# Kernel optimization log

Hardware: AMD Instinct MI355X
Metric: run time of the kernel (lower is better)

Reference implementation:

```python
import jax, jax.numpy as jnp
import numpy as np

N, E, F_IN, HID, H, NCLS, L = 100000, 1600000, 128, 128, 4, 40, 2
C = HID // H  # per-head channels = 32
LN_EPS = 1e-5
SOFTMAX_EPS = 1e-16  # PyG softmax denominator epsilon


def setup_inputs() -> dict:
    key = jax.random.key(0)
    ks = jax.random.split(key, 8)
    s = 1.0 / np.sqrt(F_IN).astype(np.float32)
    return {
        "x": jax.random.normal(ks[0], (N, F_IN), jnp.float32),
        "edge_index": jax.random.randint(ks[1], (2, E), 0, N, jnp.int32),
        "Wq": jax.random.normal(ks[2], (L, F_IN, HID), jnp.float32) * s,
        "bq": jnp.zeros((L, HID), jnp.float32),
        "Wk": jax.random.normal(ks[3], (L, F_IN, HID), jnp.float32) * s,
        "bk": jnp.zeros((L, HID), jnp.float32),
        "Wv": jax.random.normal(ks[4], (L, F_IN, HID), jnp.float32) * s,
        "bv": jnp.zeros((L, HID), jnp.float32),
        "Ws": jax.random.normal(ks[5], (L, F_IN, HID), jnp.float32) * s,
        "bs": jnp.zeros((L, HID), jnp.float32),
        "gamma": jnp.ones((L, HID), jnp.float32),
        "beta": jnp.zeros((L, HID), jnp.float32),
        "Wout": jax.random.normal(ks[6], (HID, NCLS), jnp.float32) * (1.0 / np.sqrt(HID).astype(np.float32)),
        "bout": jnp.zeros((NCLS,), jnp.float32),
    }


def _transformer_conv(x, src, dst, Wq, bq, Wk, bk, Wv, bv, Ws, bs):
    # PyG TransformerConv, concat=False, root_weight=True, beta=False
    n = x.shape[0]
    q = (x @ Wq + bq).reshape(n, H, C)
    k = (x @ Wk + bk).reshape(n, H, C)
    v = (x @ Wv + bv).reshape(n, H, C)
    # per-edge attention logits: [E, H]
    alpha = jnp.einsum('ehc,ehc->eh', q[dst], k[src]) / np.sqrt(C).astype(np.float32)
    # segment softmax over incoming edges of each destination node
    amax = jax.ops.segment_max(alpha, dst, num_segments=n)        # [N, H]
    ex = jnp.exp(alpha - amax[dst])                               # [E, H]
    denom = jax.ops.segment_sum(ex, dst, num_segments=n)         # [N, H]
    w = ex / (denom[dst] + SOFTMAX_EPS)                           # [E, H]
    msg = v[src] * w[:, :, None]                                  # [E, H, C]
    out = jax.ops.segment_sum(msg, dst, num_segments=n)          # [N, H, C]
    out = out.mean(axis=1)                                        # concat=False -> head average, [N, C*?]. Here C*H==HID only via mean over H of C dims -> [N, C]
    # NOTE: concat=False averages heads -> [N, C]; skip proj maps in->C? In PyG, out_channels=hidden here,
    # so lin_* are Linear(in, heads*hidden)... but TransformerConv(in, hidden) means out_channels=hidden/?
    return out


def _conv(x, src, dst, Wq, bq, Wk, bk, Wv, bv, Ws, bs):
    # Faithful version with out_channels = HID per head? No: TransformerConv(in, hidden, heads, concat=False)
    # in PyG uses out_channels=hidden and lin_* : in -> heads*out_channels. To keep HID total width we model
    # per-head dim C = HID // H (standard multi-head factorization with same total width HID).
    n = x.shape[0]
    q = (x @ Wq + bq).reshape(n, H, C)
    k = (x @ Wk + bk).reshape(n, H, C)
    v = (x @ Wv + bv).reshape(n, H, C)
    alpha = jnp.einsum('ehc,ehc->eh', q[dst], k[src]) / np.sqrt(C).astype(np.float32)
    amax = jax.ops.segment_max(alpha, dst, num_segments=n)
    ex = jnp.exp(alpha - amax[dst])
    denom = jax.ops.segment_sum(ex, dst, num_segments=n)
    w = ex / (denom[dst] + SOFTMAX_EPS)
    msg = (v[src] * w[:, :, None]).reshape(-1, H * C)             # [E, HID]
    agg = jax.ops.segment_sum(msg, dst, num_segments=n)          # [N, HID]
    # concat=False -> mean over heads, then broadcast back is not what PyG does; PyG yields [N, out_channels].
    out = agg.reshape(n, H, C).mean(axis=1)                       # [N, C]
    out = jnp.tile(out, (1, H))                                   # widen back to HID? No — instead use skip of width HID.
    return out


def _conv_layer(x, src, dst, Wq, bq, Wk, bk, Wv, bv, Ws, bs):
    """TransformerConv(in, HID, heads=H, concat=False): lin_{q,k,v}: in -> H*HID is too wide for a
    memory target, so we use the equivalent standard factorization HID = H*C (per-head C), giving
    attention output [N, H, C]; concat=False head-mean is applied per head group and the result is
    projected residually via lin_skip (in -> HID)."""
    n = x.shape[0]
    q = (x @ Wq + bq).reshape(n, H, C)
    k = (x @ Wk + bk).reshape(n, H, C)
    v = (x @ Wv + bv).reshape(n, H, C)
    alpha = jnp.einsum('ehc,ehc->eh', q[dst], k[src]) / np.sqrt(C).astype(np.float32)
    amax = jax.ops.segment_max(alpha, dst, num_segments=n)        # [N, H]
    ex = jnp.exp(alpha - amax[dst])                               # [E, H]
    denom = jax.ops.segment_sum(ex, dst, num_segments=n)
    w = ex / (denom[dst] + SOFTMAX_EPS)
    msg = (v[src] * w[:, :, None]).reshape(-1, HID)               # [E, HID] (head-concat)
    agg = jax.ops.segment_sum(msg, dst, num_segments=n)          # [N, HID]
    return agg + x @ Ws + bs                                      # root/skip connection


def _layernorm(h, g, b):
    mu = h.mean(-1, keepdims=True)
    var = ((h - mu) ** 2).mean(-1, keepdims=True)
    return (h - mu) * jax.lax.rsqrt(var + LN_EPS) * g + b


def reference(x, edge_index, Wq, bq, Wk, bk, Wv, bv, Ws, bs, gamma, beta, Wout, bout):
    src, dst = edge_index[0], edge_index[1]
    h = x
    for l in range(L):  # fixed small layer count
        h = _conv_layer(h, src, dst, Wq[l], bq[l], Wk[l], bk[l], Wv[l], bv[l], Ws[l], bs[l])
        h = jax.nn.relu(_layernorm(h, gamma[l], beta[l]))
        # dropout is identity in eval mode
    return h @ Wout + bout  # [N, NCLS]
```

## Files before the change

### kernel.cpp

```cpp
#include <hip/hip_runtime.h>
#include <math.h>

#define N_NODES 100000
#define N_EDGES 1600000
#define NCLS_ 40
#define NSCAN_BLOCKS ((N_NODES + 1023) / 1024)
#define DRANGE 12500
#define SRCS_PAD (N_EDGES + 3 * N_NODES + 64)

#define QSCALE (0.17677669529663687f * 1.4426950408889634f)

#if __has_builtin(__builtin_amdgcn_exp2f)
#define EXP2(x) __builtin_amdgcn_exp2f(x)
#else
#define EXP2(x) exp2f(x)
#endif

typedef short bf16x8 __attribute__((ext_vector_type(8)));
typedef float f32x4 __attribute__((ext_vector_type(4)));

__device__ __forceinline__ unsigned short f2b(float f) {
    union { float f; unsigned u; } v; v.f = f;
    unsigned r = v.u + 0x7fffu + ((v.u >> 16) & 1u);
    return (unsigned short)(r >> 16);
}
__device__ __forceinline__ unsigned cvtpk(float x, float y) {
    unsigned r;
    asm("v_cvt_pk_bf16_f32 %0, %1, %2" : "=v"(r) : "v"(x), "v"(y));
    return r;
}
__device__ __forceinline__ float2 up2(unsigned u) {
    union { unsigned u; float f; } a, b;
    a.u = u << 16; b.u = u & 0xffff0000u;
    return make_float2(a.f, b.f);
}
__device__ __forceinline__ float b2f(unsigned short s) {
    union { unsigned u; float f; } v; v.u = ((unsigned)s) << 16;
    return v.f;
}


__global__ void zero_i32_kernel(int* __restrict__ p, int n) {
    int i = blockIdx.x * blockDim.x + threadIdx.x;
    if (i < n) p[i] = 0;
}

__global__ __launch_bounds__(256) void wconv_kernel(
    const float* __restrict__ Wq, const float* __restrict__ Wk,
    const float* __restrict__ Wv, const float* __restrict__ Ws,
    unsigned short* __restrict__ Wbf) {
    int tid = blockIdx.x * 256 + threadIdx.x;
    if (tid >= 131072) return;
    int j     = tid & 7;
    int lane  = (tid >> 3) & 63;
    int ks    = (tid >> 9) & 3;
    int c     = (tid >> 11) & 3;
    int ghalf = (tid >> 13) & 1;
    int mat   = (tid >> 14) & 3;
    int l     = tid >> 16;
    int ln = lane & 15, quad = lane >> 4;
    int col = ghalf * 64 + ((ln >> 2) << 4) + (c << 2) + (ln & 3);
    int krow = (ks << 5) + (quad << 3) + j;
    const float* W = (mat == 0) ? Wq : (mat == 1) ? Wk : (mat == 2) ? Wv : Ws;
    float w = W[l * 16384 + krow * 128 + col];
    if (mat == 0) w *= QSCALE;
    Wbf[tid] = f2b(w);
}

__global__ __launch_bounds__(256) void hist_kernel(
    const int* __restrict__ dst, int* __restrict__ deg) {
    int group = blockIdx.x & 7;
    int gblk  = blockIdx.x >> 3;
    int nblk  = gridDim.x >> 3;
    int lo = group * DRANGE, hi = lo + DRANGE;
    for (int i = gblk * 256 + threadIdx.x; i < N_EDGES; i += nblk * 256) {
        int d = dst[i];
        if (d >= lo && d < hi) atomicAdd(&deg[d], 1);
    }
}

__global__ __launch_bounds__(1024) void scan_block_kernel(
    const int* __restrict__ deg, int* __restrict__ rowptr, int* __restrict__ sums) {
    __shared__ int tmp[1024];
    int t = threadIdx.x;
    int i = blockIdx.x * 1024 + t;
    int v = (i < N_NODES) ? ((deg[i] + 3) & ~3) : 0;
    tmp[t] = v;
    __syncthreads();
    for (int d = 1; d < 1024; d <<= 1) {
        int add = (t >= d) ? tmp[t - d] : 0;
        __syncthreads();
        tmp[t] += add;
        __syncthreads();
    }
    if (i < N_NODES) rowptr[i] = tmp[t] - v;
    if (t == 1023) sums[blockIdx.x] = tmp[1023];
}

__global__ __launch_bounds__(128) void scan_sums_kernel(int* __restrict__ sums) {
    __shared__ int tmp[128];
    int t = threadIdx.x;
    int v = (t < NSCAN_BLOCKS) ? sums[t] : 0;
    tmp[t] = v;
    __syncthreads();
    for (int d = 1; d < 128; d <<= 1) {
        int add = (t >= d) ? tmp[t - d] : 0;
        __syncthreads();
        tmp[t] += add;
        __syncthreads();
    }
    if (t < NSCAN_BLOCKS) sums[t] = tmp[t] - v;
}

__global__ void scan_add_kernel(int* __restrict__ rowptr, const int* __restrict__ sums,
                                const int* __restrict__ deg,
                                int* __restrict__ cursor, int* __restrict__ srcs) {
    int i = blockIdx.x * blockDim.x + threadIdx.x;
    if (i < N_NODES) {
        int val = rowptr[i] + sums[i >> 10];
        rowptr[i] = val;
        cursor[i] = val;
        int d = deg[i];
        int pad = ((d + 3) & ~3);
        for (int j = d; j < pad; ++j) srcs[val + j] = 0;
        if (i == N_NODES - 1) {
            int end = val + pad;
            for (int j = 0; j < 16; ++j) srcs[end + j] = 0;
        }
    }
}

__global__ __launch_bounds__(256) void scatter_kernel(
    const int* __restrict__ src, const int* __restrict__ dst,
    int* __restrict__ cursor, int* __restrict__ srcs) {
    int group = blockIdx.x & 7;
    int gblk  = blockIdx.x >> 3;
    int nblk  = gridDim.x >> 3;
    int lo = group * DRANGE, hi = lo + DRANGE;
    for (int i = gblk * 256 + threadIdx.x; i < N_EDGES; i += nblk * 256) {
        int d = dst[i];
        if (d >= lo && d < hi) {
            int pos = atomicAdd(&cursor[d], 1);
            srcs[pos] = src[i] << 10;
        }
    }
}

__global__ __launch_bounds__(512, 4) void gemm_qkvs_kernel(
    const void* __restrict__ Ap, int a_is_bf16,
    const unsigned short* __restrict__ Wbf,
    const float* __restrict__ b0, const float* __restrict__ b1,
    const float* __restrict__ b2, const float* __restrict__ b3,
    unsigned short* __restrict__ out) {
    __shared__ unsigned short WL[2][8192];
    int t = threadIdx.x;
    int row0 = blockIdx.x * 128;
    int wr = t >> 6, lane = t & 63;
    int ln = lane & 15, quad = lane >> 4;
    int node = row0 + wr * 16 + ln;
    int nodeC = (node < N_NODES) ? node : (N_NODES - 1);

    bf16x8 aF[4];
    if (a_is_bf16) {
        const unsigned short* ar = (const unsigned short*)Ap + (size_t)nodeC * 128;
        #pragma unroll
        for (int ks = 0; ks < 4; ++ks)
            aF[ks] = *(const bf16x8*)&ar[ks * 32 + quad * 8];
    } else {
        const float* ar = (const float*)Ap + (size_t)nodeC * 128;
        #pragma unroll
        for (int ks = 0; ks < 4; ++ks) {
            float4 f0 = *(const float4*)&ar[ks * 32 + quad * 8];
            float4 f1 = *(const float4*)&ar[ks * 32 + quad * 8 + 4];
            union { unsigned u[4]; bf16x8 v; } cv;
            cv.u[0] = cvtpk(f0.x, f0.y);
            cv.u[1] = cvtpk(f0.z, f0.w);
            cv.u[2] = cvtpk(f1.x, f1.y);
            cv.u[3] = cvtpk(f1.z, f1.w);
            aF[ks] = cv.v;
        }
    }

    {
        const uint4* Wg4 = (const uint4*)Wbf;
        uint4 a = Wg4[t * 2], b = Wg4[t * 2 + 1];
        uint4* d4 = (uint4*)WL[0] + t * 2;
        d4[0] = a; d4[1] = b;
    }
    __syncthreads();

    bool ok = node < N_NODES;
    #pragma unroll
    for (int g = 0; g < 8; ++g) {
        int mat = g >> 1;
        int cur = g & 1;
        const float* bias = (mat == 0) ? b0 : (mat == 1) ? b1 : (mat == 2) ? b2 : b3;
        int cb = (g & 1) * 64;

        uint4 pfa, pfb;
        if (g < 7) {
            const uint4* Wg4 = (const uint4*)(Wbf + (size_t)(g + 1) * 8192);
            pfa = Wg4[t * 2]; pfb = Wg4[t * 2 + 1];
        }

        f32x4 acc[4];
        #pragma unroll
        for (int c = 0; c < 4; ++c) acc[c] = (f32x4){0.f, 0.f, 0.f, 0.f};
        #pragma unroll
        for (int ks = 0; ks < 4; ++ks) {
            #pragma unroll
            for (int c = 0; c < 4; ++c) {
                bf16x8 w = *(bf16x8*)&WL[cur][((c * 4 + ks) * 64 + lane) * 8];
                acc[c] = __builtin_amdgcn_mfma_f32_16x16x32_bf16(w, aF[ks], acc[c], 0, 0, 0);
            }
        }

        if (ok) {
            float s = (mat == 0) ? QSCALE : 1.0f;
            float v[16];
            #pragma unroll
            for (int c = 0; c < 4; ++c) {
                float4 bb = *(const float4*)&bias[cb + quad * 16 + c * 4];
                v[c * 4 + 0] = acc[c][0] + bb.x * s;
                v[c * 4 + 1] = acc[c][1] + bb.y * s;
                v[c * 4 + 2] = acc[c][2] + bb.z * s;
                v[c * 4 + 3] = acc[c][3] + bb.w * s;
            }
            unsigned pk[8];
            #pragma unroll
            for (int m = 0; m < 8; ++m) pk[m] = cvtpk(v[2 * m], v[2 * m + 1]);
            unsigned short* orow = out + (size_t)node * 512;
            if (mat == 0 || mat == 3) {
                int base = (mat == 0 ? 0 : 384) + cb + quad * 16;
                uint4 w0 = make_uint4(pk[0], pk[1], pk[2], pk[3]);
                uint4 w1 = make_uint4(pk[4], pk[5], pk[6], pk[7]);
                *(uint4*)&orow[base] = w0;
                *(uint4*)&orow[base + 8] = w1;
            } else {
                int boff = (mat == 2) ? 4 : 0;
                #pragma unroll
                for (int c = 0; c < 4; ++c) {
                    int pos = 128 + 8 * ((cb >> 2) + quad * 4 + c) + boff;
                    uint2 wd; wd.x = pk[2 * c]; wd.y = pk[2 * c + 1];
                    *(uint2*)&orow[pos] = wd;
                }
            }
        }

        if (g < 7) {
            uint4* d4 = (uint4*)WL[cur ^ 1] + t * 2;
            d4[0] = pfa; d4[1] = pfb;
        }
        __syncthreads();
    }
}

#define EDGE(KV, ECOND) {                                            \
        float2 k01 = up2(KV.x), k23 = up2(KV.y);                     \
        float p = q01.x*k01.x + q01.y*k01.y + q23.x*k23.x + q23.y*k23.y; \
        p += __shfl_xor(p, 1);                                       \
        p += __shfl_xor(p, 2);                                       \
        p += __shfl_xor(p, 4);                                       \
        float e = (ECOND);                                           \
        float2 v01 = up2(KV.z), v23 = up2(KV.w);                     \
        a0 = fmaf(e, v01.x, a0); a1 = fmaf(e, v01.y, a1);            \
        a2 = fmaf(e, v23.x, a2); a3 = fmaf(e, v23.y, a3);            \
        dsum += e; }

__global__ __launch_bounds__(256) void edge_fused_kernel(
    const unsigned short* __restrict__ qkvs,
    const int* __restrict__ srcs, const int* __restrict__ rowptr,
    const int* __restrict__ deg,
    const float* __restrict__ gamma, const float* __restrict__ beta,
    unsigned short* __restrict__ hout) {
    int n = (blockIdx.x * 256 + threadIdx.x) >> 6;
    int lane = threadIdx.x & 63;
    if (n >= N_NODES) return;
    int half = lane >> 5, hl = lane & 31;
    const unsigned short* qrow = qkvs + (size_t)n * 512;
    uint2 qu = *(const uint2*)&qrow[4 * hl];
    float2 q01 = up2(qu.x), q23 = up2(qu.y);
    uint2 su = *(const uint2*)&qrow[384 + 4 * hl];
    float2 sk01 = up2(su.x), sk23 = up2(su.y);
    int e0 = rowptr[n];
    int rem = deg[n];
    const char* kbase = (const char*)qkvs + 256 + 16 * hl;
    const int* sb = srcs + e0 + 4 * half;
    float a0 = 0.f, a1 = 0.f, a2 = 0.f, a3 = 0.f, dsum = 0.f;

    int4 oc;
    if (rem >= 8) oc = *(const int4*)sb;
    while (rem >= 8) {
        int4 on;
        if (rem >= 16) on = *(const int4*)(sb + 8);
        uint4 kv0 = *(const uint4*)(kbase + (unsigned)oc.x);
        uint4 kv1 = *(const uint4*)(kbase + (unsigned)oc.y);
        uint4 kv2 = *(const uint4*)(kbase + (unsigned)oc.z);
        uint4 kv3 = *(const uint4*)(kbase + (unsigned)oc.w);
        EDGE(kv0, EXP2(p));
        EDGE(kv1, EXP2(p));
        EDGE(kv2, EXP2(p));
        EDGE(kv3, EXP2(p));
        oc = on; sb += 8; rem -= 8;
    }
    if (rem > 0) {
        int4 ot = *(const int4*)sb;
        int tb = 4 * half;
        uint4 kv0 = *(const uint4*)(kbase + (unsigned)ot.x);
        uint4 kv1 = *(const uint4*)(kbase + (unsigned)ot.y);
        uint4 kv2 = *(const uint4*)(kbase + (unsigned)ot.z);
        uint4 kv3 = *(const uint4*)(kbase + (unsigned)ot.w);
        EDGE(kv0, (tb + 0 < rem) ? EXP2(p) : 0.f);
        EDGE(kv1, (tb + 1 < rem) ? EXP2(p) : 0.f);
        EDGE(kv2, (tb + 2 < rem) ? EXP2(p) : 0.f);
        EDGE(kv3, (tb + 3 < rem) ? EXP2(p) : 0.f);
    }

    a0 += __shfl_xor(a0, 32); a1 += __shfl_xor(a1, 32);
    a2 += __shfl_xor(a2, 32); a3 += __shfl_xor(a3, 32);
    dsum += __shfl_xor(dsum, 32);
    float dinv = 1.0f / (dsum + 1e-16f);
    float o0 = a0 * dinv + sk01.x, o1 = a1 * dinv + sk01.y;
    float o2 = a2 * dinv + sk23.x, o3 = a3 * dinv + sk23.y;
    float sum = o0 + o1 + o2 + o3;
    for (int m = 1; m < 64; m <<= 1) sum += __shfl_xor(sum, m);
    float mu = sum * (1.0f / 256.0f);
    float d0 = o0 - mu, d1 = o1 - mu, d2 = o2 - mu, d3 = o3 - mu;
    float sq = d0 * d0 + d1 * d1 + d2 * d2 + d3 * d3;
    for (int m = 1; m < 64; m <<= 1) sq += __shfl_xor(sq, m);
    float rs = rsqrtf(sq * (1.0f / 256.0f) + 1e-5f);
    if (half == 0) {
        float4 g4 = *(const float4*)&gamma[4 * hl];
        float4 b4 = *(const float4*)&beta[4 * hl];
        float r0 = fmaxf(d0 * rs * g4.x + b4.x, 0.f);
        float r1 = fmaxf(d1 * rs * g4.y + b4.y, 0.f);
        float r2 = fmaxf(d2 * rs * g4.z + b4.z, 0.f);
        float r3 = fmaxf(d3 * rs * g4.w + b4.w, 0.f);
        uint2 w;
        w.x = cvtpk(r0, r1);
        w.y = cvtpk(r2, r3);
        *(uint2*)&hout[(size_t)n * 128 + 4 * hl] = w;
    }
}

__global__ __launch_bounds__(256) void out_gemm_kernel(
    const unsigned short* __restrict__ h, const float* __restrict__ Wout,
    const float* __restrict__ bout, float* __restrict__ out) {
    int wv = __builtin_amdgcn_readfirstlane((int)(threadIdx.x >> 6));
    int l = threadIdx.x & 63;
    int n = blockIdx.x * 64 + l;
    int jb = wv * 10;
    int nc = (n < N_NODES) ? n : (N_NODES - 1);
    const unsigned short* hrow = h + (size_t)nc * 128;
    uint4 hp[16];
    #pragma unroll
    for (int i = 0; i < 16; ++i) hp[i] = *(const uint4*)&hrow[i * 8];
    float acc[10];
    #pragma unroll
    for (int j = 0; j < 10; ++j) acc[j] = bout[jb + j];
    #pragma unroll
    for (int i = 0; i < 16; ++i) {
        float2 c01 = up2(hp[i].x), c23 = up2(hp[i].y);
        float2 c45 = up2(hp[i].z), c67 = up2(hp[i].w);
        float hc0 = c01.x, hc1 = c01.y, hc2 = c23.x, hc3 = c23.y;
        float hc4 = c45.x, hc5 = c45.y, hc6 = c67.x, hc7 = c67.y;
        #pragma unroll
        for (int j = 0; j < 10; ++j) {
            const float* wk = Wout + (i * 8) * NCLS_ + jb + j;
            acc[j] = fmaf(hc0, wk[0 * NCLS_], acc[j]);
            acc[j] = fmaf(hc1, wk[1 * NCLS_], acc[j]);
            acc[j] = fmaf(hc2, wk[2 * NCLS_], acc[j]);
            acc[j] = fmaf(hc3, wk[3 * NCLS_], acc[j]);
            acc[j] = fmaf(hc4, wk[4 * NCLS_], acc[j]);
            acc[j] = fmaf(hc5, wk[5 * NCLS_], acc[j]);
            acc[j] = fmaf(hc6, wk[6 * NCLS_], acc[j]);
            acc[j] = fmaf(hc7, wk[7 * NCLS_], acc[j]);
        }
    }
    if (n < N_NODES) {
        #pragma unroll
        for (int j = 0; j < 10; ++j) out[(size_t)n * NCLS_ + jb + j] = acc[j];
    }
}

extern "C" void kernel_launch(void* const* d_in, const int* in_sizes, int n_in,
                              void* d_out, int out_size, void* d_ws, size_t ws_size,
                              hipStream_t stream) {
    const float* x    = (const float*)d_in[0];
    const int*   ei   = (const int*)d_in[1];
    const int*   src  = ei;
    const int*   dst  = ei + N_EDGES;
    const float* Wq   = (const float*)d_in[2];
    const float* bq   = (const float*)d_in[3];
    const float* Wk   = (const float*)d_in[4];
    const float* bk   = (const float*)d_in[5];
    const float* Wv   = (const float*)d_in[6];
    const float* bv   = (const float*)d_in[7];
    const float* Wsk  = (const float*)d_in[8];
    const float* bsk  = (const float*)d_in[9];
    const float* gmm  = (const float*)d_in[10];
    const float* bta  = (const float*)d_in[11];
    const float* Wout = (const float*)d_in[12];
    const float* bout = (const float*)d_in[13];
    float* outp = (float*)d_out;

    char* p = (char*)d_ws;
    auto carve = [&](size_t bytes) {
        char* r = p;
        p += (bytes + 255) & ~(size_t)255;
        return r;
    };
    unsigned short* qkvs = (unsigned short*)carve((size_t)N_NODES * 512 * 2);
    unsigned short* h    = (unsigned short*)carve((size_t)N_NODES * 128 * 2);
    unsigned short* Wbf  = (unsigned short*)carve((size_t)131072 * 2);
    int* deg     = (int*)carve((size_t)N_NODES * 4);
    int* rowptr  = (int*)carve((size_t)(N_NODES + 1) * 4);
    int* cursor  = (int*)carve((size_t)N_NODES * 4);
    int* srcs    = (int*)carve((size_t)SRCS_PAD * 4);
    int* sums    = (int*)carve((size_t)NSCAN_BLOCKS * 4);

    wconv_kernel<<<512, 256, 0, stream>>>(Wq, Wk, Wv, Wsk, Wbf);

    zero_i32_kernel<<<(N_NODES + 255) / 256, 256, 0, stream>>>(deg, N_NODES);
    hist_kernel<<<2048, 256, 0, stream>>>(dst, deg);
    scan_block_kernel<<<NSCAN_BLOCKS, 1024, 0, stream>>>(deg, rowptr, sums);
    scan_sums_kernel<<<1, 128, 0, stream>>>(sums);
    scan_add_kernel<<<(N_NODES + 255) / 256, 256, 0, stream>>>(rowptr, sums, deg, cursor, srcs);
    scatter_kernel<<<2048, 256, 0, stream>>>(src, dst, cursor, srcs);

    for (int l = 0; l < 2; ++l) {
        const void* hin = l ? (const void*)h : (const void*)x;
        gemm_qkvs_kernel<<<(N_NODES + 127) / 128, 512, 0, stream>>>(
            hin, l, Wbf + (size_t)l * 65536,
            bq + l * 128, bk + l * 128, bv + l * 128, bsk + l * 128, qkvs);
        edge_fused_kernel<<<(N_NODES + 3) / 4, 256, 0, stream>>>(
            qkvs, srcs, rowptr, deg, gmm + l * 128, bta + l * 128, h);
    }
    out_gemm_kernel<<<(N_NODES + 63) / 64, 256, 0, stream>>>(h, Wout, bout, outp);
}
```

Measured before the change: 671.8 us.

## Fuse setup kernels and drop range-partitioned atomics in CSR build

```diff
diff --git a/kernel.cpp b/kernel.cpp
--- a/kernel.cpp
+++ b/kernel.cpp
@@ -5,7 +5,6 @@
 #define N_EDGES 1600000
 #define NCLS_ 40
 #define NSCAN_BLOCKS ((N_NODES + 1023) / 1024)
-#define DRANGE 12500
 #define SRCS_PAD (N_EDGES + 3 * N_NODES + 64)
 
 #define QSCALE (0.17677669529663687f * 1.4426950408889634f)
@@ -40,17 +39,17 @@
 }
 
 
-__global__ void zero_i32_kernel(int* __restrict__ p, int n) {
-    int i = blockIdx.x * blockDim.x + threadIdx.x;
-    if (i < n) p[i] = 0;
-}
-
-__global__ __launch_bounds__(256) void wconv_kernel(
+__global__ __launch_bounds__(256) void wconv_zero_kernel(
     const float* __restrict__ Wq, const float* __restrict__ Wk,
     const float* __restrict__ Wv, const float* __restrict__ Ws,
-    unsigned short* __restrict__ Wbf) {
-    int tid = blockIdx.x * 256 + threadIdx.x;
-    if (tid >= 131072) return;
+    unsigned short* __restrict__ Wbf, int* __restrict__ deg) {
+    int b = blockIdx.x;
+    if (b >= 512) {
+        int i = (b - 512) * 256 + threadIdx.x;
+        if (i < N_NODES) deg[i] = 0;
+        return;
+    }
+    int tid = b * 256 + threadIdx.x;
     int j     = tid & 7;
     int lane  = (tid >> 3) & 63;
     int ks    = (tid >> 9) & 3;
@@ -69,14 +68,9 @@
 
 __global__ __launch_bounds__(256) void hist_kernel(
     const int* __restrict__ dst, int* __restrict__ deg) {
-    int group = blockIdx.x & 7;
-    int gblk  = blockIdx.x >> 3;
-    int nblk  = gridDim.x >> 3;
-    int lo = group * DRANGE, hi = lo + DRANGE;
-    for (int i = gblk * 256 + threadIdx.x; i < N_EDGES; i += nblk * 256) {
-        int d = dst[i];
-        if (d >= lo && d < hi) atomicAdd(&deg[d], 1);
-    }
+    int stride = gridDim.x * 256;
+    for (int i = blockIdx.x * 256 + threadIdx.x; i < N_EDGES; i += stride)
+        atomicAdd(&deg[dst[i]], 1);
 }
 
 __global__ __launch_bounds__(1024) void scan_block_kernel(
@@ -97,27 +91,25 @@
     if (t == 1023) sums[blockIdx.x] = tmp[1023];
 }
 
-__global__ __launch_bounds__(128) void scan_sums_kernel(int* __restrict__ sums) {
-    __shared__ int tmp[128];
+__global__ __launch_bounds__(256) void scan_add_kernel(
+    int* __restrict__ rowptr, const int* __restrict__ sums,
+    const int* __restrict__ deg,
+    int* __restrict__ cursor, int* __restrict__ srcs) {
+    __shared__ int base_s;
     int t = threadIdx.x;
-    int v = (t < NSCAN_BLOCKS) ? sums[t] : 0;
-    tmp[t] = v;
+    int limit = blockIdx.x >> 2;
+    if (t < 64) {
+        int v = (t < limit) ? sums[t] : 0;
+        int v2 = (t + 64 < limit) ? sums[t + 64] : 0;
+        v += v2;
+        for (int m = 1; m < 64; m <<= 1) v += __shfl_xor(v, m);
+        if (t == 0) base_s = v;
+    }
     __syncthreads();
-    for (int d = 1; d < 128; d <<= 1) {
-        int add = (t >= d) ? tmp[t - d] : 0;
-        __syncthreads();
-        tmp[t] += add;
-        __syncthreads();
-    }
-    if (t < NSCAN_BLOCKS) sums[t] = tmp[t] - v;
-}
-
-__global__ void scan_add_kernel(int* __restrict__ rowptr, const int* __restrict__ sums,
-                                const int* __restrict__ deg,
-                                int* __restrict__ cursor, int* __restrict__ srcs) {
-    int i = blockIdx.x * blockDim.x + threadIdx.x;
+    int base = base_s;
+    int i = blockIdx.x * 256 + t;
     if (i < N_NODES) {
-        int val = rowptr[i] + sums[i >> 10];
+        int val = rowptr[i] + base;
         rowptr[i] = val;
         cursor[i] = val;
         int d = deg[i];
@@ -133,16 +125,10 @@
 __global__ __launch_bounds__(256) void scatter_kernel(
     const int* __restrict__ src, const int* __restrict__ dst,
     int* __restrict__ cursor, int* __restrict__ srcs) {
-    int group = blockIdx.x & 7;
-    int gblk  = blockIdx.x >> 3;
-    int nblk  = gridDim.x >> 3;
-    int lo = group * DRANGE, hi = lo + DRANGE;
-    for (int i = gblk * 256 + threadIdx.x; i < N_EDGES; i += nblk * 256) {
-        int d = dst[i];
-        if (d >= lo && d < hi) {
-            int pos = atomicAdd(&cursor[d], 1);
-            srcs[pos] = src[i] << 10;
-        }
+    int stride = gridDim.x * 256;
+    for (int i = blockIdx.x * 256 + threadIdx.x; i < N_EDGES; i += stride) {
+        int pos = atomicAdd(&cursor[dst[i]], 1);
+        srcs[pos] = src[i] << 10;
     }
 }
 
@@ -419,12 +405,10 @@
     int* srcs    = (int*)carve((size_t)SRCS_PAD * 4);
     int* sums    = (int*)carve((size_t)NSCAN_BLOCKS * 4);
 
-    wconv_kernel<<<512, 256, 0, stream>>>(Wq, Wk, Wv, Wsk, Wbf);
-
-    zero_i32_kernel<<<(N_NODES + 255) / 256, 256, 0, stream>>>(deg, N_NODES);
+    wconv_zero_kernel<<<512 + (N_NODES + 255) / 256, 256, 0, stream>>>(
+        Wq, Wk, Wv, Wsk, Wbf, deg);
     hist_kernel<<<2048, 256, 0, stream>>>(dst, deg);
     scan_block_kernel<<<NSCAN_BLOCKS, 1024, 0, stream>>>(deg, rowptr, sums);
-    scan_sums_kernel<<<1, 128, 0, stream>>>(sums);
     scan_add_kernel<<<(N_NODES + 255) / 256, 256, 0, stream>>>(rowptr, sums, deg, cursor, srcs);
     scatter_kernel<<<2048, 256, 0, stream>>>(src, dst, cursor, srcs);
 
```

Measured after the change: 692.0 us. 1.03x slower.
